# Kernel tuning notes

Hardware: AMD Instinct MI355X
Metric: run time of the kernel (lower is better)

## Reference

```python
import jax, jax.numpy as jnp
import numpy as np

B, S, H, D = 2, 2048, 16, 128
HID = H * D
THETA = 10000.0
SCALE = 1.0 / np.sqrt(D)


def setup_inputs() -> dict:
    key = jax.random.key(0)
    k1, k2, k3 = jax.random.split(key, 3)
    x = jax.random.normal(k1, (B, S, HID), dtype=jnp.float32)
    w_qkv = jax.random.normal(k2, (3 * HID, HID), dtype=jnp.float32) * 0.02
    w_o = jax.random.normal(k3, (HID, HID), dtype=jnp.float32) * 0.02
    return {"x": x, "w_qkv": w_qkv, "w_o": w_o}


def _rope_cos_sin(seq_len, dim, dtype):
    inv_freq = 1.0 / (THETA ** (jnp.arange(0, dim, 2, dtype=jnp.float32) / dim))
    pos = jnp.arange(seq_len, dtype=jnp.float32)
    freqs = pos[:, None] * inv_freq[None, :]          # (S, D/2)
    emb = jnp.concatenate([freqs, freqs], axis=-1)    # (S, D)
    return jnp.cos(emb).astype(dtype), jnp.sin(emb).astype(dtype)


def _rotate_half(t):
    t1, t2 = jnp.split(t, 2, axis=-1)
    return jnp.concatenate([-t2, t1], axis=-1)


def reference(x, w_qkv, w_o):
    b, s, _ = x.shape
    qkv = jnp.einsum('bsh,oh->bso', x, w_qkv)                 # (B,S,3*HID)
    qkv = qkv.reshape(b, s, 3, H, D).transpose(2, 0, 3, 1, 4)  # (3,B,H,S,D)
    q, k, v = qkv[0], qkv[1], qkv[2]
    cos, sin = _rope_cos_sin(s, D, x.dtype)                    # (S,D)
    q = q * cos + _rotate_half(q) * sin
    k = k * cos + _rotate_half(k) * sin
    scores = jnp.einsum('bhqd,bhkd->bhqk', q, k) * SCALE       # (B,H,S,S)
    causal = jnp.triu(jnp.ones((s, s), dtype=bool), k=1)
    scores = jnp.where(causal[None, None], -jnp.inf, scores)
    attn = jax.nn.softmax(scores.astype(jnp.float32), axis=-1).astype(q.dtype)
    out = jnp.einsum('bhqk,bhkd->bhqd', attn, v)               # (B,H,S,D)
    out = out.transpose(0, 2, 1, 3).reshape(b, s, HID)
    return jnp.einsum('bsh,oh->bso', out, w_o)
```

## Files before the change

kernel.cpp:

```cpp
#include <hip/hip_runtime.h>
#include <hip/hip_bf16.h>

typedef unsigned short u16;
typedef unsigned long long u64;
typedef u16 us8 __attribute__((ext_vector_type(8)));
typedef __bf16 bf8_t __attribute__((ext_vector_type(8)));
typedef float f32x4 __attribute__((ext_vector_type(4)));

__device__ __forceinline__ float b2f(u16 u) {
    return __uint_as_float(((unsigned int)u) << 16);
}
__device__ __forceinline__ u16 f2b(float f) {
    union { __hip_bfloat16 h; u16 u; } v;
    v.h = __float2bfloat16(f);
    return v.u;
}
__device__ __forceinline__ f32x4 mfma16(bf8_t a, bf8_t b, f32x4 c) {
    return __builtin_amdgcn_mfma_f32_16x16x32_bf16(a, b, c, 0, 0, 0);
}
__device__ __forceinline__ void gload_lds16(const u16* g, u16* lds_base) {
    __builtin_amdgcn_global_load_lds((const __attribute__((address_space(1))) unsigned int*)g,
                                     (__attribute__((address_space(3))) unsigned int*)lds_base,
                                     16, 0, 0);
}

__global__ __launch_bounds__(256) void f32_to_bf16(const float* __restrict__ src,
                                                   u16* __restrict__ dst, int n8) {
    int idx = blockIdx.x * 256 + threadIdx.x;
    if (idx >= n8) return;
    float4 f0 = ((const float4*)src)[idx * 2];
    float4 f1 = ((const float4*)src)[idx * 2 + 1];
    us8 o;
    o[0] = f2b(f0.x); o[1] = f2b(f0.y); o[2] = f2b(f0.z); o[3] = f2b(f0.w);
    o[4] = f2b(f1.x); o[5] = f2b(f1.y); o[6] = f2b(f1.z); o[7] = f2b(f1.w);
    ((us8*)dst)[idx] = o;
}

template<int STORE_F32>
__global__ __launch_bounds__(256) void gemm_mfma_bt(const u16* __restrict__ A, const u16* __restrict__ B,
                                                    void* __restrict__ Cout, int M, int N, int K, int ldc) {
    __shared__ u16 Alds[128 * 32];
    __shared__ u16 Blds[128 * 32];
    const int tid = threadIdx.x;
    const int lane = tid & 63, wave = tid >> 6;
    const int lm = lane & 15, lq = lane >> 4;
    const int wm = wave >> 1, wn = wave & 1;
    const int m0 = blockIdx.y * 128, n0 = blockIdx.x * 128;
    const int srow = lane >> 2;
    const int scol = (lane & 3) * 8;

    f32x4 acc[4][4] = {};

    for (int k0 = 0; k0 < K; k0 += 32) {
#pragma unroll
        for (int p = 0; p < 2; p++) {
            int rbase = wave * 16 + p * 64;
            gload_lds16(A + (size_t)(m0 + rbase + srow) * K + k0 + scol, &Alds[rbase * 32]);
            gload_lds16(B + (size_t)(n0 + rbase + srow) * K + k0 + scol, &Blds[rbase * 32]);
        }
        __syncthreads();
        bf8_t af[4], bf[4];
#pragma unroll
        for (int mb = 0; mb < 4; mb++)
            af[mb] = *(const bf8_t*)&Alds[(wm * 64 + mb * 16 + lm) * 32 + lq * 8];
#pragma unroll
        for (int nb = 0; nb < 4; nb++)
            bf[nb] = *(const bf8_t*)&Blds[(wn * 64 + nb * 16 + lm) * 32 + lq * 8];
#pragma unroll
        for (int mb = 0; mb < 4; mb++)
#pragma unroll
            for (int nb = 0; nb < 4; nb++)
                acc[mb][nb] = mfma16(af[mb], bf[nb], acc[mb][nb]);
        __syncthreads();
    }
#pragma unroll
    for (int mb = 0; mb < 4; mb++)
#pragma unroll
        for (int nb = 0; nb < 4; nb++)
#pragma unroll
            for (int r = 0; r < 4; r++) {
                int row = m0 + wm * 64 + mb * 16 + lq * 4 + r;
                int col = n0 + wn * 64 + nb * 16 + lm;
                if (STORE_F32)
                    ((float*)Cout)[(size_t)row * ldc + col] = acc[mb][nb][r];
                else
                    ((u16*)Cout)[(size_t)row * ldc + col] = f2b(acc[mb][nb][r]);
            }
}

__global__ __launch_bounds__(256) void rope_vt(u16* __restrict__ qkv, u16* __restrict__ VT) {
    __shared__ u16 T[64 * 136];
    const int tid = threadIdx.x;
    const int s0 = blockIdx.x * 64;
    const int bh = blockIdx.y;
    const int b = bh >> 4, h = bh & 15;
#pragma unroll
    for (int p = 0; p < 4; p++) {
        int sl = p * 16 + (tid >> 4);
        int d0 = (tid & 15) * 8;
        *(us8*)&T[sl * 136 + d0] =
            *(const us8*)(qkv + ((size_t)(b * 2048 + s0 + sl)) * 6144 + 4096 + h * 128 + d0);
    }
#pragma unroll
    for (int p = 0; p < 2; p++) {
        int task = p * 256 + tid;
        int sl = task >> 3;
        int jg = task & 7;
        size_t base = ((size_t)(b * 2048 + s0 + sl)) * 6144 + h * 128 + jg * 8;
        us8 qlo = *(const us8*)(qkv + base);
        us8 qhi = *(const us8*)(qkv + base + 64);
        us8 klo = *(const us8*)(qkv + base + 2048);
        us8 khi = *(const us8*)(qkv + base + 2048 + 64);
        us8 oql, oqh, okl, okh;
        float s = (float)(s0 + sl);
#pragma unroll
        for (int e = 0; e < 8; e++) {
            int j = jg * 8 + e;
            float inv = __expf((float)j * (-9.210340371976184f / 64.f));
            float ang = s * inv;
            float sn, c;
            __sincosf(ang, &sn, &c);
            float q1 = b2f(qlo[e]), q2 = b2f(qhi[e]);
            oql[e] = f2b(q1 * c - q2 * sn);
            oqh[e] = f2b(q2 * c + q1 * sn);
            float k1 = b2f(klo[e]), k2 = b2f(khi[e]);
            okl[e] = f2b(k1 * c - k2 * sn);
            okh[e] = f2b(k2 * c + k1 * sn);
        }
        *(us8*)(qkv + base) = oql;
        *(us8*)(qkv + base + 64) = oqh;
        *(us8*)(qkv + base + 2048) = okl;
        *(us8*)(qkv + base + 2048 + 64) = okh;
    }
    __syncthreads();
#pragma unroll
    for (int p = 0; p < 4; p++) {
        int idx = p * 256 + tid;
        int d = idx & 127;
        int sg = idx >> 7;
        us8 v;
#pragma unroll
        for (int i = 0; i < 8; i++) v[i] = T[(sg * 8 + i) * 136 + d];
        *(us8*)&VT[((size_t)bh * 128 + d) * 2048 + s0 + sg * 8] = v;
    }
}

#define ATT_SCALE 0.08838834764831845f

__global__ __launch_bounds__(256, 2) void attn_flash(const u16* __restrict__ qkv, const u16* __restrict__ VT,
                                                     u16* __restrict__ AO) {
    const int bh = blockIdx.x;
    const int qt = 15 - blockIdx.y;
    const int b = bh >> 4, h = bh & 15;
    const int tid = threadIdx.x, lane = tid & 63, wave = tid >> 6;
    const int lm = lane & 15, lq = lane >> 4;
    const int q0 = qt * 128;

    __shared__ u16 Kt[64 * 136];
    __shared__ u16 Vt[128 * 72];

    bf8_t qf[2][4];
#pragma unroll
    for (int qg = 0; qg < 2; qg++) {
        const u16* Qrow = qkv + ((size_t)(b * 2048 + q0 + qg * 64 + wave * 16 + lm)) * 6144 + h * 128;
#pragma unroll
        for (int ks = 0; ks < 4; ks++)
            qf[qg][ks] = *(const bf8_t*)(Qrow + ks * 32 + lq * 8);
    }

    f32x4 Of[2][8] = {};
    float mrun[2] = {-3.0e38f, -3.0e38f}, lrun[2] = {0.f, 0.f};

    const u16* Kbase = qkv + (size_t)b * 2048 * 6144 + 2048 + h * 128;
    const u16* VTbase = VT + (size_t)bh * 128 * 2048;

    const int krow = tid >> 4;
    const int kcol = (tid & 15) * 8;
    const int vrow = tid >> 3;
    const int vcol = (tid & 7) * 8;
    const int ktmax = 2 * qt + 1;

    us8 kreg[4], vreg[4];
#pragma unroll
    for (int p = 0; p < 4; p++) {
        kreg[p] = *(const us8*)(Kbase + (size_t)(p * 16 + krow) * 6144 + kcol);
        vreg[p] = *(const us8*)(VTbase + (size_t)(p * 32 + vrow) * 2048 + vcol);
    }

    for (int kt = 0; kt <= ktmax; kt++) {
        __syncthreads();
#pragma unroll
        for (int p = 0; p < 4; p++) {
            *(us8*)&Kt[(p * 16 + krow) * 136 + kcol] = kreg[p];
            *(us8*)&Vt[(p * 32 + vrow) * 72 + vcol] = vreg[p];
        }
        __syncthreads();
        {
            int kn = (kt + 1 <= ktmax ? kt + 1 : ktmax) * 64;
#pragma unroll
            for (int p = 0; p < 4; p++) {
                kreg[p] = *(const us8*)(Kbase + (size_t)(kn + p * 16 + krow) * 6144 + kcol);
                vreg[p] = *(const us8*)(VTbase + (size_t)(p * 32 + vrow) * 2048 + kn + vcol);
            }
        }

        u64 pk[2][4];
        float alpha[2];
#pragma unroll
        for (int qg = 0; qg < 2; qg++) {
            float sv[4][4];
#pragma unroll
            for (int nb = 0; nb < 4; nb++) {
                f32x4 a = {};
#pragma unroll
                for (int ks = 0; ks < 4; ks++) {
                    bf8_t kf = *(const bf8_t*)&Kt[(nb * 16 + lm) * 136 + ks * 32 + lq * 8];
                    a = mfma16(kf, qf[qg][ks], a);
                }
#pragma unroll
                for (int r = 0; r < 4; r++) sv[nb][r] = a[r] * ATT_SCALE;
            }
            if (kt >= 2 * qt + qg) {
                int qglob = q0 + qg * 64 + wave * 16 + lm;
#pragma unroll
                for (int nb = 0; nb < 4; nb++)
#pragma unroll
                    for (int r = 0; r < 4; r++)
                        if (kt * 64 + nb * 16 + lq * 4 + r > qglob) sv[nb][r] = -3.0e38f;
            }
            float mx = -3.0e38f;
#pragma unroll
            for (int nb = 0; nb < 4; nb++)
#pragma unroll
                for (int r = 0; r < 4; r++) mx = fmaxf(mx, sv[nb][r]);
            mx = fmaxf(mx, __shfl_xor(mx, 16, 64));
            mx = fmaxf(mx, __shfl_xor(mx, 32, 64));
            float mnew = fmaxf(mrun[qg], mx);
            float a_ = __expf(mrun[qg] - mnew);
            float rs = 0.f;
#pragma unroll
            for (int nb = 0; nb < 4; nb++) {
                float e0 = __expf(sv[nb][0] - mnew), e1 = __expf(sv[nb][1] - mnew);
                float e2 = __expf(sv[nb][2] - mnew), e3 = __expf(sv[nb][3] - mnew);
                rs += (e0 + e1) + (e2 + e3);
                unsigned int lo = (unsigned int)f2b(e0) | ((unsigned int)f2b(e1) << 16);
                unsigned int hi = (unsigned int)f2b(e2) | ((unsigned int)f2b(e3) << 16);
                pk[qg][nb] = (u64)lo | ((u64)hi << 32);
            }
            rs += __shfl_xor(rs, 16, 64);
            rs += __shfl_xor(rs, 32, 64);
            lrun[qg] = lrun[qg] * a_ + rs;
            mrun[qg] = mnew;
            alpha[qg] = a_;
#pragma unroll
            for (int db = 0; db < 8; db++)
#pragma unroll
                for (int r = 0; r < 4; r++) Of[qg][db][r] *= a_;
        }

        const int slo = ((lq & 1) * 2) * 16 + lm;
        const int shi = slo + 16;
        const bool sel = (lq >> 1) != 0;
#pragma unroll
        for (int kk = 0; kk < 2; kk++) {
            union { u64 v[2]; bf8_t f; } pf[2];
#pragma unroll
            for (int qg = 0; qg < 2; qg++) {
                u64 lo0 = __shfl(pk[qg][2 * kk + 0], slo, 64);
                u64 lo1 = __shfl(pk[qg][2 * kk + 1], slo, 64);
                u64 hi0 = __shfl(pk[qg][2 * kk + 0], shi, 64);
                u64 hi1 = __shfl(pk[qg][2 * kk + 1], shi, 64);
                pf[qg].v[0] = sel ? lo1 : lo0;
                pf[qg].v[1] = sel ? hi1 : hi0;
            }
#pragma unroll
            for (int db = 0; db < 8; db++) {
                bf8_t vf = *(const bf8_t*)&Vt[(db * 16 + lm) * 72 + kk * 32 + lq * 8];
                Of[0][db] = mfma16(vf, pf[0].f, Of[0][db]);
                Of[1][db] = mfma16(vf, pf[1].f, Of[1][db]);
            }
        }
    }
#pragma unroll
    for (int qg = 0; qg < 2; qg++) {
        float invl = 1.f / lrun[qg];
        size_t rowbase = (size_t)(b * 2048 + q0 + qg * 64 + wave * 16 + lm) * 2048 + h * 128;
#pragma unroll
        for (int db = 0; db < 8; db++) {
            ushort4 o;
            o.x = f2b(Of[qg][db][0] * invl);
            o.y = f2b(Of[qg][db][1] * invl);
            o.z = f2b(Of[qg][db][2] * invl);
            o.w = f2b(Of[qg][db][3] * invl);
            *(ushort4*)(AO + rowbase + db * 16 + lq * 4) = o;
        }
    }
}

extern "C" void kernel_launch(void* const* d_in, const int* in_sizes, int n_in,
                              void* d_out, int out_size, void* d_ws, size_t ws_size,
                              hipStream_t stream) {
    const float* x     = (const float*)d_in[0];
    const float* w_qkv = (const float*)d_in[1];
    const float* w_o   = (const float*)d_in[2];
    float* out = (float*)d_out;
    u16* ws = (u16*)d_ws;

    u16* qkvb  = ws;
    u16* VT    = ws + 25165824;
    u16* AO    = ws + 33554432;
    u16* xb    = ws + 41943040;
    u16* wqkvb = ws + 50331648;
    u16* wob   = ws + 62914560;

    f32_to_bf16<<<4096, 256, 0, stream>>>(x, xb, 1048576);
    f32_to_bf16<<<6144, 256, 0, stream>>>(w_qkv, wqkvb, 1572864);
    f32_to_bf16<<<2048, 256, 0, stream>>>(w_o, wob, 524288);
    gemm_mfma_bt<0><<<dim3(48, 32), 256, 0, stream>>>(xb, wqkvb, qkvb, 4096, 6144, 2048, 6144);
    rope_vt<<<dim3(32, 32), 256, 0, stream>>>(qkvb, VT);
    attn_flash<<<dim3(32, 16), 256, 0, stream>>>(qkvb, VT, AO);
    gemm_mfma_bt<1><<<dim3(16, 32), 256, 0, stream>>>(AO, wob, out, 4096, 2048, 2048, 2048);
}
```

Before: 422.6 us.

## Fuse RoPE into QKV GEMM epilogue, switch GEMMs to 32x32 MFMA, merge conversions

```diff
diff --git a/kernel.cpp b/kernel.cpp
--- a/kernel.cpp
+++ b/kernel.cpp
@@ -6,6 +6,7 @@
 typedef u16 us8 __attribute__((ext_vector_type(8)));
 typedef __bf16 bf8_t __attribute__((ext_vector_type(8)));
 typedef float f32x4 __attribute__((ext_vector_type(4)));
+typedef float f32x16 __attribute__((ext_vector_type(16)));
 
 __device__ __forceinline__ float b2f(u16 u) {
     return __uint_as_float(((unsigned int)u) << 16);
@@ -18,38 +19,45 @@
 __device__ __forceinline__ f32x4 mfma16(bf8_t a, bf8_t b, f32x4 c) {
     return __builtin_amdgcn_mfma_f32_16x16x32_bf16(a, b, c, 0, 0, 0);
 }
+__device__ __forceinline__ f32x16 mfma32(bf8_t a, bf8_t b, f32x16 c) {
+    return __builtin_amdgcn_mfma_f32_32x32x16_bf16(a, b, c, 0, 0, 0);
+}
 __device__ __forceinline__ void gload_lds16(const u16* g, u16* lds_base) {
     __builtin_amdgcn_global_load_lds((const __attribute__((address_space(1))) unsigned int*)g,
                                      (__attribute__((address_space(3))) unsigned int*)lds_base,
                                      16, 0, 0);
 }
 
-__global__ __launch_bounds__(256) void f32_to_bf16(const float* __restrict__ src,
-                                                   u16* __restrict__ dst, int n8) {
+__global__ __launch_bounds__(256) void cvt_all(const float* __restrict__ x, const float* __restrict__ wq,
+                                               const float* __restrict__ wo, u16* __restrict__ xb,
+                                               u16* __restrict__ wqb, u16* __restrict__ wob) {
     int idx = blockIdx.x * 256 + threadIdx.x;
-    if (idx >= n8) return;
-    float4 f0 = ((const float4*)src)[idx * 2];
-    float4 f1 = ((const float4*)src)[idx * 2 + 1];
+    const float* s; u16* d; int off;
+    if (idx < 1048576)      { s = x;  d = xb;  off = idx; }
+    else if (idx < 2621440) { s = wq; d = wqb; off = idx - 1048576; }
+    else                    { s = wo; d = wob; off = idx - 2621440; }
+    float4 f0 = ((const float4*)s)[(size_t)off * 2];
+    float4 f1 = ((const float4*)s)[(size_t)off * 2 + 1];
     us8 o;
     o[0] = f2b(f0.x); o[1] = f2b(f0.y); o[2] = f2b(f0.z); o[3] = f2b(f0.w);
     o[4] = f2b(f1.x); o[5] = f2b(f1.y); o[6] = f2b(f1.z); o[7] = f2b(f1.w);
-    ((us8*)dst)[idx] = o;
-}
-
-template<int STORE_F32>
-__global__ __launch_bounds__(256) void gemm_mfma_bt(const u16* __restrict__ A, const u16* __restrict__ B,
-                                                    void* __restrict__ Cout, int M, int N, int K, int ldc) {
+    ((us8*)d)[off] = o;
+}
+
+#define ROPE_COEF (-0.14391156514261285f)
+template<int MODE>
+__global__ __launch_bounds__(256) void gemm32(const u16* __restrict__ A, const u16* __restrict__ B,
+                                              void* __restrict__ Cout, int M, int N, int K, int ldc) {
     __shared__ u16 Alds[128 * 32];
     __shared__ u16 Blds[128 * 32];
     const int tid = threadIdx.x;
     const int lane = tid & 63, wave = tid >> 6;
-    const int lm = lane & 15, lq = lane >> 4;
-    const int wm = wave >> 1, wn = wave & 1;
+    const int l31 = lane & 31, kg = lane >> 5;
     const int m0 = blockIdx.y * 128, n0 = blockIdx.x * 128;
     const int srow = lane >> 2;
     const int scol = (lane & 3) * 8;
 
-    f32x4 acc[4][4] = {};
+    f32x16 acc[4] = {};
 
     for (int k0 = 0; k0 < K; k0 += 32) {
 #pragma unroll
@@ -59,36 +67,64 @@
             gload_lds16(B + (size_t)(n0 + rbase + srow) * K + k0 + scol, &Blds[rbase * 32]);
         }
         __syncthreads();
-        bf8_t af[4], bf[4];
-#pragma unroll
-        for (int mb = 0; mb < 4; mb++)
-            af[mb] = *(const bf8_t*)&Alds[(wm * 64 + mb * 16 + lm) * 32 + lq * 8];
+        bf8_t af[2];
+#pragma unroll
+        for (int ks = 0; ks < 2; ks++)
+            af[ks] = *(const bf8_t*)&Alds[(wave * 32 + l31) * 32 + ks * 16 + kg * 8];
+        bf8_t bfr[4][2];
 #pragma unroll
         for (int nb = 0; nb < 4; nb++)
-            bf[nb] = *(const bf8_t*)&Blds[(wn * 64 + nb * 16 + lm) * 32 + lq * 8];
-#pragma unroll
-        for (int mb = 0; mb < 4; mb++)
+#pragma unroll
+            for (int ks = 0; ks < 2; ks++)
+                bfr[nb][ks] = *(const bf8_t*)&Blds[(nb * 32 + l31) * 32 + ks * 16 + kg * 8];
+#pragma unroll
+        for (int ks = 0; ks < 2; ks++)
 #pragma unroll
             for (int nb = 0; nb < 4; nb++)
-                acc[mb][nb] = mfma16(af[mb], bf[nb], acc[mb][nb]);
+                acc[nb] = mfma32(af[ks], bfr[nb][ks], acc[nb]);
         __syncthreads();
     }
-#pragma unroll
-    for (int mb = 0; mb < 4; mb++)
+
+    if (MODE == 0) {
+        int type = blockIdx.x >> 4;
+        if (type < 2) {
+#pragma unroll
+            for (int nb = 0; nb < 2; nb++) {
+                float j = (float)(nb * 32 + l31);
+                float inv = __expf(j * ROPE_COEF);
+#pragma unroll
+                for (int r = 0; r < 16; r++) {
+                    int rl = wave * 32 + (r & 3) + 8 * (r >> 2) + 4 * kg;
+                    int s = (m0 + rl) & 2047;
+                    float sn, c;
+                    __sincosf((float)s * inv, &sn, &c);
+                    float x1 = acc[nb][r], x2 = acc[nb + 2][r];
+                    acc[nb][r]     = x1 * c - x2 * sn;
+                    acc[nb + 2][r] = x2 * c + x1 * sn;
+                }
+            }
+        }
+        u16* Co = (u16*)Cout;
 #pragma unroll
         for (int nb = 0; nb < 4; nb++)
 #pragma unroll
-            for (int r = 0; r < 4; r++) {
-                int row = m0 + wm * 64 + mb * 16 + lq * 4 + r;
-                int col = n0 + wn * 64 + nb * 16 + lm;
-                if (STORE_F32)
-                    ((float*)Cout)[(size_t)row * ldc + col] = acc[mb][nb][r];
-                else
-                    ((u16*)Cout)[(size_t)row * ldc + col] = f2b(acc[mb][nb][r]);
-            }
-}
-
-__global__ __launch_bounds__(256) void rope_vt(u16* __restrict__ qkv, u16* __restrict__ VT) {
+            for (int r = 0; r < 16; r++) {
+                int rl = wave * 32 + (r & 3) + 8 * (r >> 2) + 4 * kg;
+                Co[(size_t)(m0 + rl) * ldc + n0 + nb * 32 + l31] = f2b(acc[nb][r]);
+            }
+    } else {
+        float* Co = (float*)Cout;
+#pragma unroll
+        for (int nb = 0; nb < 4; nb++)
+#pragma unroll
+            for (int r = 0; r < 16; r++) {
+                int rl = wave * 32 + (r & 3) + 8 * (r >> 2) + 4 * kg;
+                Co[(size_t)(m0 + rl) * ldc + n0 + nb * 32 + l31] = acc[nb][r];
+            }
+    }
+}
+
+__global__ __launch_bounds__(256) void transpose_v(const u16* __restrict__ qkv, u16* __restrict__ VT) {
     __shared__ u16 T[64 * 136];
     const int tid = threadIdx.x;
     const int s0 = blockIdx.x * 64;
@@ -100,37 +136,6 @@
         int d0 = (tid & 15) * 8;
         *(us8*)&T[sl * 136 + d0] =
             *(const us8*)(qkv + ((size_t)(b * 2048 + s0 + sl)) * 6144 + 4096 + h * 128 + d0);
-    }
-#pragma unroll
-    for (int p = 0; p < 2; p++) {
-        int task = p * 256 + tid;
-        int sl = task >> 3;
-        int jg = task & 7;
-        size_t base = ((size_t)(b * 2048 + s0 + sl)) * 6144 + h * 128 + jg * 8;
-        us8 qlo = *(const us8*)(qkv + base);
-        us8 qhi = *(const us8*)(qkv + base + 64);
-        us8 klo = *(const us8*)(qkv + base + 2048);
-        us8 khi = *(const us8*)(qkv + base + 2048 + 64);
-        us8 oql, oqh, okl, okh;
-        float s = (float)(s0 + sl);
-#pragma unroll
-        for (int e = 0; e < 8; e++) {
-            int j = jg * 8 + e;
-            float inv = __expf((float)j * (-9.210340371976184f / 64.f));
-            float ang = s * inv;
-            float sn, c;
-            __sincosf(ang, &sn, &c);
-            float q1 = b2f(qlo[e]), q2 = b2f(qhi[e]);
-            oql[e] = f2b(q1 * c - q2 * sn);
-            oqh[e] = f2b(q2 * c + q1 * sn);
-            float k1 = b2f(klo[e]), k2 = b2f(khi[e]);
-            okl[e] = f2b(k1 * c - k2 * sn);
-            okh[e] = f2b(k2 * c + k1 * sn);
-        }
-        *(us8*)(qkv + base) = oql;
-        *(us8*)(qkv + base + 64) = oqh;
-        *(us8*)(qkv + base + 2048) = okl;
-        *(us8*)(qkv + base + 2048 + 64) = okh;
     }
     __syncthreads();
 #pragma unroll
@@ -205,7 +210,6 @@
         }
 
         u64 pk[2][4];
-        float alpha[2];
 #pragma unroll
         for (int qg = 0; qg < 2; qg++) {
             float sv[4][4];
@@ -251,7 +255,6 @@
             rs += __shfl_xor(rs, 32, 64);
             lrun[qg] = lrun[qg] * a_ + rs;
             mrun[qg] = mnew;
-            alpha[qg] = a_;
 #pragma unroll
             for (int db = 0; db < 8; db++)
 #pragma unroll
@@ -313,11 +316,9 @@
     u16* wqkvb = ws + 50331648;
     u16* wob   = ws + 62914560;
 
-    f32_to_bf16<<<4096, 256, 0, stream>>>(x, xb, 1048576);
-    f32_to_bf16<<<6144, 256, 0, stream>>>(w_qkv, wqkvb, 1572864);
-    f32_to_bf16<<<2048, 256, 0, stream>>>(w_o, wob, 524288);
-    gemm_mfma_bt<0><<<dim3(48, 32), 256, 0, stream>>>(xb, wqkvb, qkvb, 4096, 6144, 2048, 6144);
-    rope_vt<<<dim3(32, 32), 256, 0, stream>>>(qkvb, VT);
+    cvt_all<<<12288, 256, 0, stream>>>(x, w_qkv, w_o, xb, wqkvb, wob);
+    gemm32<0><<<dim3(48, 32), 256, 0, stream>>>(xb, wqkvb, qkvb, 4096, 6144, 2048, 6144);
+    transpose_v<<<dim3(32, 32), 256, 0, stream>>>(qkvb, VT);
     attn_flash<<<dim3(32, 16), 256, 0, stream>>>(qkvb, VT, AO);
-    gemm_mfma_bt<1><<<dim3(16, 32), 256, 0, stream>>>(AO, wob, out, 4096, 2048, 2048, 2048);
-}
+    gemm32<1><<<dim3(16, 32), 256, 0, stream>>>(AO, wob, out, 4096, 2048, 2048, 2048);
+}
```

New measurement: 451.7 us. 6.9% more time.
